# Kernel optimization log

Measured on AMD Instinct MI355X. Metric: run time of the kernel, lower is better.

Reference implementation:

```python
import jax, jax.numpy as jnp
import numpy as np

N, M = 8192, 1024  # n_frames, feature dim (input_size == output_size == 1024)
Q_SCALE = 0.06
DROP_P = 0.5


def setup_inputs() -> dict:
    key = jax.random.key(0)
    kx, kk, kq, kv, ko, ku = jax.random.split(key, 6)
    w_std = 0.02
    return {
        "x": jax.random.normal(kx, (N, M), dtype=jnp.float32),
        # nn.Linear stores weight as [out_features, in_features]
        "Wk": jax.random.normal(kk, (M, M), dtype=jnp.float32) * w_std,
        "Wq": jax.random.normal(kq, (M, M), dtype=jnp.float32) * w_std,
        "Wv": jax.random.normal(kv, (M, M), dtype=jnp.float32) * w_std,
        "Wo": jax.random.normal(ko, (M, M), dtype=jnp.float32) * w_std,
        # uniform noise for dropout mask on the [N, N] attention matrix
        "u": jax.random.uniform(ku, (N, N), dtype=jnp.float32),
    }


def reference(x, Wk, Wq, Wv, Wo, u):
    # projections (bias-free Linear: y = x @ W.T)
    K = x @ Wk.T                      # [N, M]
    Q = (x @ Wq.T) * Q_SCALE          # [N, M], Q *= 0.06
    V = x @ Wv.T                      # [N, M]
    logits = Q @ K.T                  # [N, N]
    attn = jax.nn.softmax(logits, axis=-1)
    # Dropout(p=0.5) in train mode: keep with prob 0.5, scale by 1/(1-p)=2
    keep = jnp.where(u >= DROP_P, jnp.float32(1.0 / (1.0 - DROP_P)), jnp.float32(0.0))
    w = attn * keep                   # [N, N]
    y = w @ V                         # [N, M]
    return y @ Wo.T                   # [N, M]
```

## Files before the change

### kernel.cpp

```cpp
#include <hip/hip_runtime.h>
#include <cstdint>
#include <cstddef>

#define NFRAMES 8192
#define MDIM    1024
#define Q_SCALE 0.06f

#define BM 256
#define BN 128
#define BK 64

typedef __bf16 bf16x8 __attribute__((ext_vector_type(8)));
typedef float  f32x4  __attribute__((ext_vector_type(4)));
typedef unsigned short us8 __attribute__((ext_vector_type(8)));

__device__ __forceinline__ unsigned short f2bf(float f) {
  union { float f; uint32_t u; } a; a.f = f;
  uint32_t u = a.u;
  u += 0x7FFFu + ((u >> 16) & 1u);
  return (unsigned short)(u >> 16);
}
__device__ __forceinline__ float bf2f(unsigned short h) {
  union { uint32_t u; float f; } a; a.u = ((uint32_t)h) << 16; return a.f;
}

__device__ __forceinline__ void async_ld16(const void* g, void* l) {
  __builtin_amdgcn_global_load_lds(
      (const __attribute__((address_space(1))) void*)(uintptr_t)g,
      (__attribute__((address_space(3))) void*)(uint32_t)(uintptr_t)l,
      16, 0, 0);
}

__device__ __forceinline__ void store_val(float* p, float v) { *p = v; }
__device__ __forceinline__ void store_val(unsigned short* p, float v) { *p = f2bf(v); }

template <typename OutT>
__global__ __launch_bounds__(512, 2) void gemm_bt8(
    const unsigned short* __restrict__ A, int lda,
    const unsigned short* __restrict__ B, int ldb,
    OutT* __restrict__ C, int ldc, int K)
{
  __shared__ alignas(16) unsigned short As[3 * BM * BK];
  __shared__ alignas(16) unsigned short Bs[3 * BN * BK];

  const int tid  = threadIdx.x;
  const int wave = tid >> 6;
  const int lane = tid & 63;

  const int gX  = (int)gridDim.x;
  const int nwg = gX * (int)gridDim.y;
  const int L   = (int)blockIdx.y * gX + (int)blockIdx.x;
  const int qq  = nwg >> 3;
  const int Ls  = (L & 7) * qq + (L >> 3);
  const int bx  = Ls % gX, by = Ls / gX;

  const int m0 = by * BM, n0 = bx * BN;
  const int wm = (wave >> 1) * 64;
  const int wn = (wave & 1) * 64;
  const int fr = lane & 15, fq = lane >> 4;

  const int l8 = lane >> 3, l7 = lane & 7;
  const size_t ldaB = (size_t)lda * 2, ldbB = (size_t)ldb * 2;
  const char* aSrc = (const char*)A + (size_t)(m0 + wave * 8 + l8) * ldaB + ((l7 ^ l8) << 4);
  const char* bSrc = (const char*)B + (size_t)(n0 + wave * 8 + l8) * ldbB + ((l7 ^ l8) << 4);
  unsigned short* aDst = As + wave * 512;
  unsigned short* bDst = Bs + wave * 512;

  const int xorv = (fr & 7) << 4;
  const int cA0 = (fq * 16) ^ xorv;
  const int cA1 = (64 + fq * 16) ^ xorv;
  const char* aRd = (const char*)As + (wm + fr) * 128;
  const char* bRd = (const char*)Bs + (wn + fr) * 128;

  f32x4 acc[4][4] = {};
  const int NT = K >> 6;

#define STA(buf, s, t) async_ld16(aSrc + (size_t)((s) * 64) * ldaB + (size_t)(t) * 128, \
                                  aDst + (buf) * 16384 + (s) * 4096)
#define STB(buf, s, t) async_ld16(bSrc + (size_t)((s) * 64) * ldbB + (size_t)(t) * 128, \
                                  bDst + (buf) * 8192 + (s) * 4096)

  STA(0, 0, 0); STA(0, 1, 0); STA(0, 2, 0); STA(0, 3, 0); STB(0, 0, 0); STB(0, 1, 0);
  if (NT > 1) { STA(1, 0, 1); STA(1, 1, 1); STA(1, 2, 1); STA(1, 3, 1); STB(1, 0, 1); STB(1, 1, 1); }
  asm volatile("s_waitcnt vmcnt(6)" ::: "memory");
  __builtin_amdgcn_s_barrier();

  for (int t = 0; t < NT; ++t) {
    const int cur = t % 3;
    const int u   = t + 2;
    const int ub  = u % 3;
    const bool st = (u < NT);
    const char* aB = aRd + cur * 32768;
    const char* bB = bRd + cur * 16384;

    bf16x8 bh[4][2];
#pragma unroll
    for (int j = 0; j < 4; ++j) {
      bh[j][0] = *(const bf16x8*)(bB + j * 2048 + cA0);
      bh[j][1] = *(const bf16x8*)(bB + j * 2048 + cA1);
    }
    bf16x8 a0[2][2];
#pragma unroll
    for (int i = 0; i < 2; ++i) {
      a0[i][0] = *(const bf16x8*)(aB + i * 2048 + cA0);
      a0[i][1] = *(const bf16x8*)(aB + i * 2048 + cA1);
    }
    if (st) { STA(ub, 0, u); STA(ub, 1, u); STB(ub, 0, u); }
    __builtin_amdgcn_s_barrier();
    asm volatile("s_waitcnt lgkmcnt(0)" ::: "memory");
    __builtin_amdgcn_sched_barrier(0);
    __builtin_amdgcn_s_setprio(1);
#pragma unroll
    for (int kk = 0; kk < 2; ++kk)
#pragma unroll
      for (int i = 0; i < 2; ++i)
#pragma unroll
        for (int j = 0; j < 4; ++j)
          acc[i][j] = __builtin_amdgcn_mfma_f32_16x16x32_bf16(
              kk ? a0[i][1] : a0[i][0], kk ? bh[j][1] : bh[j][0], acc[i][j], 0, 0, 0);
    __builtin_amdgcn_s_setprio(0);
    __builtin_amdgcn_s_barrier();

    bf16x8 a1[2][2];
#pragma unroll
    for (int i = 0; i < 2; ++i) {
      a1[i][0] = *(const bf16x8*)(aB + (2 + i) * 2048 + cA0);
      a1[i][1] = *(const bf16x8*)(aB + (2 + i) * 2048 + cA1);
    }
    if (st) { STA(ub, 2, u); STA(ub, 3, u); STB(ub, 1, u); }
    if (st) { asm volatile("s_waitcnt vmcnt(6)" ::: "memory"); }
    else    { asm volatile("s_waitcnt vmcnt(0)" ::: "memory"); }
    __builtin_amdgcn_s_barrier();
    asm volatile("s_waitcnt lgkmcnt(0)" ::: "memory");
    __builtin_amdgcn_sched_barrier(0);
    __builtin_amdgcn_s_setprio(1);
#pragma unroll
    for (int kk = 0; kk < 2; ++kk)
#pragma unroll
      for (int i = 0; i < 2; ++i)
#pragma unroll
        for (int j = 0; j < 4; ++j)
          acc[2 + i][j] = __builtin_amdgcn_mfma_f32_16x16x32_bf16(
              kk ? a1[i][1] : a1[i][0], kk ? bh[j][1] : bh[j][0], acc[2 + i][j], 0, 0, 0);
    __builtin_amdgcn_s_setprio(0);
    __builtin_amdgcn_s_barrier();
  }
#undef STA
#undef STB

#pragma unroll
  for (int i = 0; i < 4; ++i)
#pragma unroll
    for (int j = 0; j < 4; ++j)
#pragma unroll
      for (int r = 0; r < 4; ++r) {
        int row = m0 + wm + i * 16 + fq * 4 + r;
        int col = n0 + wn + j * 16 + fr;
        store_val(&C[(size_t)row * ldc + col], acc[i][j][r]);
      }
}

__global__ __launch_bounds__(256) void softmax_dropout_kernel(
    const unsigned short* __restrict__ S, const float* __restrict__ U,
    unsigned short* __restrict__ P)
{
  const int row = blockIdx.x;
  const us8*   s8 = (const us8*)(S + (size_t)row * NFRAMES);
  const f32x4* u4 = (const f32x4*)(U + (size_t)row * NFRAMES);
  us8*         p8 = (us8*)(P + (size_t)row * NFRAMES);
  const int tid = threadIdx.x;
  const int lane = tid & 63, wave = tid >> 6;

  float v[32];
  float mx = -3.4e38f;
#pragma unroll
  for (int j = 0; j < 4; ++j) {
    us8 t = __builtin_nontemporal_load(s8 + j * 256 + tid);
#pragma unroll
    for (int e = 0; e < 8; ++e) {
      float f = bf2f(t[e]);
      v[j * 8 + e] = f;
      mx = fmaxf(mx, f);
    }
  }
#pragma unroll
  for (int o = 32; o > 0; o >>= 1) mx = fmaxf(mx, __shfl_xor(mx, o));
  __shared__ float redm[4];
  __shared__ float reds[4];
  if (lane == 0) redm[wave] = mx;
  __syncthreads();
  mx = fmaxf(fmaxf(redm[0], redm[1]), fmaxf(redm[2], redm[3]));

  float sum = 0.f;
#pragma unroll
  for (int i = 0; i < 32; ++i) { v[i] = __expf(v[i] - mx); sum += v[i]; }
#pragma unroll
  for (int o = 32; o > 0; o >>= 1) sum += __shfl_xor(sum, o);
  if (lane == 0) reds[wave] = sum;
  __syncthreads();
  sum = reds[0] + reds[1] + reds[2] + reds[3];
  float inv = 1.0f / sum;

#pragma unroll
  for (int j = 0; j < 4; ++j) {
    f32x4 ua = __builtin_nontemporal_load(u4 + (j * 256 + tid) * 2);
    f32x4 ub = __builtin_nontemporal_load(u4 + (j * 256 + tid) * 2 + 1);
    us8 o;
    o[0] = f2bf(v[j*8+0] * inv * (ua[0] >= 0.5f ? 2.0f : 0.0f));
    o[1] = f2bf(v[j*8+1] * inv * (ua[1] >= 0.5f ? 2.0f : 0.0f));
    o[2] = f2bf(v[j*8+2] * inv * (ua[2] >= 0.5f ? 2.0f : 0.0f));
    o[3] = f2bf(v[j*8+3] * inv * (ua[3] >= 0.5f ? 2.0f : 0.0f));
    o[4] = f2bf(v[j*8+4] * inv * (ub[0] >= 0.5f ? 2.0f : 0.0f));
    o[5] = f2bf(v[j*8+5] * inv * (ub[1] >= 0.5f ? 2.0f : 0.0f));
    o[6] = f2bf(v[j*8+6] * inv * (ub[2] >= 0.5f ? 2.0f : 0.0f));
    o[7] = f2bf(v[j*8+7] * inv * (ub[3] >= 0.5f ? 2.0f : 0.0f));
    p8[j * 256 + tid] = o;
  }
}

__device__ __forceinline__ void cvt4(const float* in, unsigned short* out, int i, float s) {
  float4 t = ((const float4*)in)[i];
  ushort4 o;
  o.x = f2bf(t.x * s); o.y = f2bf(t.y * s); o.z = f2bf(t.z * s); o.w = f2bf(t.w * s);
  ((ushort4*)out)[i] = o;
}

__global__ __launch_bounds__(256) void cvt_all(
    const float* __restrict__ x, const float* __restrict__ Wk,
    const float* __restrict__ Wq, const float* __restrict__ Wv,
    const float* __restrict__ Wo,
    unsigned short* __restrict__ xb, unsigned short* __restrict__ wkq,
    unsigned short* __restrict__ wvb, unsigned short* __restrict__ wob)
{
  int i = blockIdx.x * 256 + threadIdx.x;
  const int XSZ = (NFRAMES * MDIM) / 4;
  const int WSZ = (MDIM * MDIM) / 4;
  if (i < XSZ) { cvt4(x, xb, i, 1.0f); return; }
  i -= XSZ;
  if (i < WSZ) { cvt4(Wk, wkq, i, 1.0f); return; }
  i -= WSZ;
  if (i < WSZ) { cvt4(Wq, wkq + MDIM * MDIM, i, Q_SCALE); return; }
  i -= WSZ;
  if (i < WSZ) { cvt4(Wv, wvb, i, 1.0f); return; }
  i -= WSZ;
  if (i < WSZ) { cvt4(Wo, wob, i, 1.0f); return; }
}

extern "C" void kernel_launch(void* const* d_in, const int* in_sizes, int n_in,
                              void* d_out, int out_size, void* d_ws, size_t ws_size,
                              hipStream_t stream) {
  const float* x  = (const float*)d_in[0];
  const float* Wk = (const float*)d_in[1];
  const float* Wq = (const float*)d_in[2];
  const float* Wv = (const float*)d_in[3];
  const float* Wo = (const float*)d_in[4];
  const float* u  = (const float*)d_in[5];
  float* out = (float*)d_out;

  const int N = NFRAMES, M = MDIM;
  char* base = (char*)d_ws;
  size_t off = 0;
  auto alloc = [&](size_t bytes) -> void* {
    void* p = base + off; off += (bytes + 255) & ~(size_t)255; return p;
  };
  unsigned short* xb  = (unsigned short*)alloc((size_t)N * M * 2);
  unsigned short* wkq = (unsigned short*)alloc((size_t)2 * M * M * 2);
  unsigned short* wvb = (unsigned short*)alloc((size_t)M * M * 2);
  unsigned short* wob = (unsigned short*)alloc((size_t)M * M * 2);
  unsigned short* KQb = (unsigned short*)alloc((size_t)N * 2 * M * 2);
  unsigned short* Vt  = (unsigned short*)alloc((size_t)M * N * 2);
  unsigned short* yb  = (unsigned short*)alloc((size_t)N * M * 2);

  size_t avail = ws_size > off ? ws_size - off : 0;
  int R = 256;
  const int cands[6] = {8192, 4096, 2048, 1024, 512, 256};
  for (int ci = 0; ci < 6; ++ci) {
    size_t need = (size_t)cands[ci] * N * 2 * 2 + 1024;
    if (need <= avail) { R = cands[ci]; break; }
  }
  unsigned short* Sb = (unsigned short*)alloc((size_t)R * N * 2);
  unsigned short* Pb = (unsigned short*)alloc((size_t)R * N * 2);

  {
    int total4 = (N * M + 4 * M * M) / 4;
    cvt_all<<<(total4 + 255) / 256, 256, 0, stream>>>(x, Wk, Wq, Wv, Wo, xb, wkq, wvb, wob);
  }

  gemm_bt8<unsigned short><<<dim3(2 * M / BN, N / BM), 512, 0, stream>>>(
      xb, M, wkq, M, KQb, 2 * M, M);
  gemm_bt8<unsigned short><<<dim3(N / BN, M / BM), 512, 0, stream>>>(
      wvb, M, xb, M, Vt, N, M);

  for (int i0 = 0; i0 < N; i0 += R) {
    gemm_bt8<unsigned short><<<dim3(N / BN, R / BM), 512, 0, stream>>>(
        KQb + M + (size_t)i0 * 2 * M, 2 * M,
        KQb, 2 * M,
        Sb, N, M);
    softmax_dropout_kernel<<<R, 256, 0, stream>>>(Sb, u + (size_t)i0 * N, Pb);
    gemm_bt8<unsigned short><<<dim3(M / BN, R / BM), 512, 0, stream>>>(
        Pb, N, Vt, N, yb + (size_t)i0 * M, M, N);
  }

  gemm_bt8<float><<<dim3(M / BN, N / BM), 512, 0, stream>>>(
      yb, M, wob, M, out, M, M);
}
```

Baseline: 767.1 us.

## Add 256x256-tile GEMM with split-K for PV product and reduction

Adds a new GEMM kernel with 256x256 output tiles and double-buffered LDS, used for the QK/KQ projection, the logits GEMM and the P·V GEMM. The P·V GEMM is split along K into two halves writing fp32 partials into the now-free S buffer, and a small reduce kernel sums them and converts to bf16. Larger tiles raise arithmetic intensity, and split-K restores parallelism for the narrow M=1024 output. The cost is more registers and LDS per block, an extra fp32 write/read pass, and an extra launch per chunk.

```diff
diff --git a/kernel.cpp b/kernel.cpp
--- a/kernel.cpp
+++ b/kernel.cpp
@@ -6,9 +6,11 @@
 #define MDIM    1024
 #define Q_SCALE 0.06f
 
+#define BK 64
+#define BM2 256
+#define BN2 256
 #define BM 256
 #define BN 128
-#define BK 64
 
 typedef __bf16 bf16x8 __attribute__((ext_vector_type(8)));
 typedef float  f32x4  __attribute__((ext_vector_type(4)));
@@ -33,6 +35,131 @@
 
 __device__ __forceinline__ void store_val(float* p, float v) { *p = v; }
 __device__ __forceinline__ void store_val(unsigned short* p, float v) { *p = f2bf(v); }
+
+template <typename OutT>
+__global__ __launch_bounds__(512, 2) void gemm_big(
+    const unsigned short* __restrict__ A, int lda,
+    const unsigned short* __restrict__ B, int ldb,
+    OutT* __restrict__ C, int ldc, long cz, int kChunk)
+{
+  __shared__ alignas(16) unsigned short As[2 * BM2 * BK];
+  __shared__ alignas(16) unsigned short Bs[2 * BN2 * BK];
+
+  const int tid  = threadIdx.x;
+  const int wave = tid >> 6;
+  const int lane = tid & 63;
+
+  const int gX  = (int)gridDim.x;
+  const int nwg = gX * (int)gridDim.y;
+  int bx = (int)blockIdx.x, by = (int)blockIdx.y;
+  if ((nwg & 7) == 0) {
+    const int L  = by * gX + bx;
+    const int qq = nwg >> 3;
+    const int Ls = (L & 7) * qq + (L >> 3);
+    bx = Ls % gX; by = Ls / gX;
+  }
+
+  const int m0 = by * BM2, n0 = bx * BN2;
+  const int wm = (wave >> 2) * 128;
+  const int wn = (wave & 3) * 64;
+  const int fr = lane & 15, fq = lane >> 4;
+
+  const int kOff = (int)blockIdx.z * kChunk;
+  OutT* Cz = C + (size_t)blockIdx.z * cz;
+
+  const int l8 = lane >> 3, l7 = lane & 7;
+  const size_t ldaB = (size_t)lda * 2, ldbB = (size_t)ldb * 2;
+  const char* aSrc = (const char*)A + (size_t)(m0 + wave * 8 + l8) * ldaB
+                     + (size_t)kOff * 2 + ((l7 ^ l8) << 4);
+  const char* bSrc = (const char*)B + (size_t)(n0 + wave * 8 + l8) * ldbB
+                     + (size_t)kOff * 2 + ((l7 ^ l8) << 4);
+  unsigned short* aDst = As + wave * 512;
+  unsigned short* bDst = Bs + wave * 512;
+
+  const int xorv = (fr & 7) << 4;
+  const int c0 = (fq * 16) ^ xorv;
+  const int c1 = (64 + fq * 16) ^ xorv;
+  const char* aRd = (const char*)As + (wm + fr) * 128;
+  const char* bRd = (const char*)Bs + (wn + fr) * 128;
+
+  f32x4 acc[8][4] = {};
+  const int NT = kChunk >> 6;
+
+#define STA2(buf, s, t) async_ld16(aSrc + (size_t)((s) * 64) * ldaB + (size_t)(t) * 128, \
+                                   aDst + (buf) * 16384 + (s) * 4096)
+#define STB2(buf, s, t) async_ld16(bSrc + (size_t)((s) * 64) * ldbB + (size_t)(t) * 128, \
+                                   bDst + (buf) * 16384 + (s) * 4096)
+
+  STA2(0, 0, 0); STA2(0, 1, 0); STA2(0, 2, 0); STA2(0, 3, 0);
+  STB2(0, 0, 0); STB2(0, 1, 0); STB2(0, 2, 0); STB2(0, 3, 0);
+  asm volatile("s_waitcnt vmcnt(0)" ::: "memory");
+  __builtin_amdgcn_s_barrier();
+
+  for (int t = 0; t < NT; ++t) {
+    const int cur = t & 1;
+    const bool st = (t + 1 < NT);
+    const char* aB = aRd + cur * 32768;
+    const char* bB = bRd + cur * 32768;
+
+    if (st) {
+      const int u = t + 1, ub = cur ^ 1;
+      STA2(ub, 0, u); STA2(ub, 1, u); STA2(ub, 2, u); STA2(ub, 3, u);
+      STB2(ub, 0, u); STB2(ub, 1, u); STB2(ub, 2, u); STB2(ub, 3, u);
+    }
+    __builtin_amdgcn_sched_barrier(0);
+
+    bf16x8 bh[4][2];
+#pragma unroll
+    for (int j = 0; j < 4; ++j) {
+      bh[j][0] = *(const bf16x8*)(bB + j * 2048 + c0);
+      bh[j][1] = *(const bf16x8*)(bB + j * 2048 + c1);
+    }
+    bf16x8 ar[2][2][2];
+#pragma unroll
+    for (int i = 0; i < 2; ++i) {
+      ar[0][i][0] = *(const bf16x8*)(aB + i * 2048 + c0);
+      ar[0][i][1] = *(const bf16x8*)(aB + i * 2048 + c1);
+    }
+
+#pragma unroll
+    for (int ph = 0; ph < 4; ++ph) {
+      const int pc = ph & 1, pn = pc ^ 1;
+      if (ph < 3) {
+#pragma unroll
+        for (int i = 0; i < 2; ++i) {
+          ar[pn][i][0] = *(const bf16x8*)(aB + (ph * 2 + 2 + i) * 2048 + c0);
+          ar[pn][i][1] = *(const bf16x8*)(aB + (ph * 2 + 2 + i) * 2048 + c1);
+        }
+      }
+      __builtin_amdgcn_s_setprio(1);
+#pragma unroll
+      for (int kk = 0; kk < 2; ++kk)
+#pragma unroll
+        for (int i = 0; i < 2; ++i)
+#pragma unroll
+          for (int j = 0; j < 4; ++j)
+            acc[ph * 2 + i][j] = __builtin_amdgcn_mfma_f32_16x16x32_bf16(
+                ar[pc][i][kk], bh[j][kk], acc[ph * 2 + i][j], 0, 0, 0);
+      __builtin_amdgcn_s_setprio(0);
+    }
+
+    if (st) { asm volatile("s_waitcnt vmcnt(0)" ::: "memory"); }
+    __builtin_amdgcn_s_barrier();
+  }
+#undef STA2
+#undef STB2
+
+#pragma unroll
+  for (int mf = 0; mf < 8; ++mf)
+#pragma unroll
+    for (int nf = 0; nf < 4; ++nf)
+#pragma unroll
+      for (int r = 0; r < 4; ++r) {
+        int row = m0 + wm + mf * 16 + fq * 4 + r;
+        int col = n0 + wn + nf * 16 + fr;
+        store_val(&Cz[(size_t)row * ldc + col], acc[mf][nf][r]);
+      }
+}
 
 template <typename OutT>
 __global__ __launch_bounds__(512, 2) void gemm_bt8(
@@ -246,6 +373,23 @@
   if (i < WSZ) { cvt4(Wo, wob, i, 1.0f); return; }
 }
 
+__global__ __launch_bounds__(256) void reduce2_bf16(
+    const float* __restrict__ Yp, long zs,
+    unsigned short* __restrict__ out, int n4)
+{
+  int i = blockIdx.x * 256 + threadIdx.x;
+  if (i < n4) {
+    f32x4 a = __builtin_nontemporal_load((const f32x4*)Yp + i);
+    f32x4 b = __builtin_nontemporal_load((const f32x4*)(Yp + zs) + i);
+    ushort4 o;
+    o.x = f2bf(a[0] + b[0]);
+    o.y = f2bf(a[1] + b[1]);
+    o.z = f2bf(a[2] + b[2]);
+    o.w = f2bf(a[3] + b[3]);
+    ((ushort4*)out)[i] = o;
+  }
+}
+
 extern "C" void kernel_launch(void* const* d_in, const int* in_sizes, int n_in,
                               void* d_out, int out_size, void* d_ws, size_t ws_size,
                               hipStream_t stream) {
@@ -280,25 +424,28 @@
   }
   unsigned short* Sb = (unsigned short*)alloc((size_t)R * N * 2);
   unsigned short* Pb = (unsigned short*)alloc((size_t)R * N * 2);
+  float* Yp = (float*)Sb;
 
   {
     int total4 = (N * M + 4 * M * M) / 4;
     cvt_all<<<(total4 + 255) / 256, 256, 0, stream>>>(x, Wk, Wq, Wv, Wo, xb, wkq, wvb, wob);
   }
 
-  gemm_bt8<unsigned short><<<dim3(2 * M / BN, N / BM), 512, 0, stream>>>(
-      xb, M, wkq, M, KQb, 2 * M, M);
+  gemm_big<unsigned short><<<dim3(2 * M / BN2, N / BM2), 512, 0, stream>>>(
+      xb, M, wkq, M, KQb, 2 * M, 0, M);
   gemm_bt8<unsigned short><<<dim3(N / BN, M / BM), 512, 0, stream>>>(
       wvb, M, xb, M, Vt, N, M);
 
   for (int i0 = 0; i0 < N; i0 += R) {
-    gemm_bt8<unsigned short><<<dim3(N / BN, R / BM), 512, 0, stream>>>(
+    gemm_big<unsigned short><<<dim3(N / BN2, R / BM2), 512, 0, stream>>>(
         KQb + M + (size_t)i0 * 2 * M, 2 * M,
         KQb, 2 * M,
-        Sb, N, M);
+        Sb, N, 0, M);
     softmax_dropout_kernel<<<R, 256, 0, stream>>>(Sb, u + (size_t)i0 * N, Pb);
-    gemm_bt8<unsigned short><<<dim3(M / BN, R / BM), 512, 0, stream>>>(
-        Pb, N, Vt, N, yb + (size_t)i0 * M, M, N);
+    gemm_big<float><<<dim3(M / BN2, R / BM2, 2), 512, 0, stream>>>(
+        Pb, N, Vt, N, Yp, M, (long)R * M, N / 2);
+    reduce2_bf16<<<(R * M / 4 + 255) / 256, 256, 0, stream>>>(
+        Yp, (long)R * M, yb + (size_t)i0 * M, R * M / 4);
   }
 
   gemm_bt8<float><<<dim3(M / BN, N / BM), 512, 0, stream>>>(
```

New measurement: 716.8 us. 1.07x faster.
